# Optimization experiments

Measured on AMD Instinct MI355X. Metric: run time of the kernel, lower is better.

## Reference

```python
import jax, jax.numpy as jnp
import numpy as np

GRID_SIZE = 5
GRID_RANGE = (-1.0, 1.0)


def setup_inputs() -> dict:
    key = jax.random.key(0)
    k1, k2, k3 = jax.random.split(key, 3)
    B, D, U, K = 16384, 1024, 128, GRID_SIZE + 3  # spline_order=3
    x = jax.random.normal(k1, (B, D), dtype=jnp.float32)
    # glorot-ish scale for weights
    base_weight = jax.random.normal(k2, (D, U), dtype=jnp.float32) * (1.0 / np.sqrt(D))
    spline_weight = jax.random.normal(k3, (D, U, K), dtype=jnp.float32) * (1.0 / np.sqrt(D))
    return {"x": x, "base_weight": base_weight, "spline_weight": spline_weight}


def reference(x, base_weight, spline_weight):
    # base path: SiLU(x @ W_b)
    base_out = jax.nn.silu(x @ base_weight)  # [B, U]
    # spline path: RBF over grid centers, then contract (note: x_norm in the
    # original call() is computed but unused, so it is omitted here)
    centers = jnp.linspace(GRID_RANGE[0], GRID_RANGE[1], GRID_SIZE)  # [G]
    dist = jnp.square(x[..., None] - centers)        # [B, D, G]
    rbf = jnp.exp(-5.0 * dist)                        # [B, D, G]
    spline_out = jnp.einsum('big,iug->bu', rbf, spline_weight[:, :, :GRID_SIZE])
    return base_out + spline_out
```

## Files before the change

### kernel.cpp

```cpp
#include <hip/hip_runtime.h>

typedef unsigned short u16;
typedef unsigned int u32;
typedef __bf16 bf16x8 __attribute__((ext_vector_type(8)));
typedef float f32x16 __attribute__((ext_vector_type(16)));

#define C2 (-7.213475204444817f)
#define T1C 0.28650480f
#define T2C 0.0067379470f

__device__ __forceinline__ u16 f2bf(float f) {
  u32 u = __float_as_uint(f);
  return (u16)((u + 0x7FFFu + ((u >> 16) & 1u)) >> 16);
}

__device__ __forceinline__ f32x16 mfma16(uint4 a, uint4 b, f32x16 c) {
  return __builtin_amdgcn_mfma_f32_32x32x16_bf16(
      __builtin_bit_cast(bf16x8, a), __builtin_bit_cast(bf16x8, b), c, 0, 0, 0);
}

__global__ __launch_bounds__(256) void kan_prep(const float* __restrict__ wb,
                                                const float* __restrict__ ws,
                                                u16* __restrict__ wst3) {
  __shared__ u16 tile[6][16][130];
  const int t = threadIdx.x;
  const int c = blockIdx.x;
#pragma unroll
  for (int it = 0; it < 8; ++it) {
    int idx = it * 256 + t;
    int d = idx >> 7, u = idx & 127;
    size_t base = (size_t)(c * 16 + d) * 128 + u;
    const float* p = ws + base * 8;
    float4 v0 = *(const float4*)p;
    float g4 = p[4];
    tile[0][d][u] = f2bf(v0.x);
    tile[1][d][u] = f2bf(v0.y);
    tile[2][d][u] = f2bf(v0.z);
    tile[3][d][u] = f2bf(v0.w);
    tile[4][d][u] = f2bf(g4);
    tile[5][d][u] = f2bf(wb[base]);
  }
  __syncthreads();
#pragma unroll
  for (int i = 0; i < 6; ++i) {
    int g = i * 256 + t;
    int s = g >> 8, r = g & 255;
    int nq = r >> 6, l = r & 63;
    int u = nq * 32 + (l & 31);
    int dbase = (l >> 5) * 8;
    u32 q[4];
#pragma unroll
    for (int j = 0; j < 4; ++j) {
      u32 lo = tile[s][dbase + 2 * j][u];
      u32 hi = tile[s][dbase + 2 * j + 1][u];
      q[j] = lo | (hi << 16);
    }
    uint4 w4; w4.x = q[0]; w4.y = q[1]; w4.z = q[2]; w4.w = q[3];
    *(uint4*)(wst3 + (size_t)c * 12288 + (size_t)g * 8) = w4;
  }
}

__global__ __launch_bounds__(512, 2) void kan_main(const float* __restrict__ x,
                                                   const u16* __restrict__ wst3,
                                                   float* __restrict__ out) {
  __shared__ __align__(16) char lds[98304];

  const int t = threadIdx.x;
  const int lane = t & 63;
  const int w = t >> 6;
  const int b0 = blockIdx.x * 64;

  if (w < 4) {
    const int pid = (w << 6) + lane;
    const int r0 = pid >> 3;
    const int o = pid & 7;
    const u32 aw0 = ((u32)(o >> 1) << 10) + ((u32)(o & 1) << 9) +
                    ((u32)((r0 ^ o) & 31) << 4);
    const u32 aw1 = aw0 + 4096;
    const float* xpA = x + (size_t)(b0 + r0) * 1024 + o * 8;
    const float* xpB = xpA + 32 * 1024;

    auto rbf6 = [&](char* buf, u32 aw, float4 xa, float4 xb) {
      float xf[8] = {xa.x, xa.y, xa.z, xa.w, xb.x, xb.y, xb.z, xb.w};
      u32 pk[6][4];
#pragma unroll
      for (int pp = 0; pp < 4; ++pp) {
        u32 lo6[6], hi6[6];
#pragma unroll
        for (int e = 0; e < 2; ++e) {
          float xv = xf[2 * pp + e];
          float t0 = C2 * xv;
          float P = __builtin_amdgcn_exp2f(t0 * xv);
          float Qp = __builtin_amdgcn_exp2f(-t0);
          float Qm = __builtin_amdgcn_exp2f(t0);
          float PQ = P * Qp, PQm = P * Qm;
          u32* dst = e ? hi6 : lo6;
          dst[0] = __float_as_uint(PQm * Qm * T2C) + 0x8000u;
          dst[1] = __float_as_uint(PQm * T1C) + 0x8000u;
          dst[2] = __float_as_uint(P) + 0x8000u;
          dst[3] = __float_as_uint(PQ * T1C) + 0x8000u;
          dst[4] = __float_as_uint(PQ * Qp * T2C) + 0x8000u;
          dst[5] = __float_as_uint(xv) + 0x8000u;
        }
#pragma unroll
        for (int s = 0; s < 6; ++s)
          pk[s][pp] = __builtin_amdgcn_perm(hi6[s], lo6[s], 0x07060302);
      }
#pragma unroll
      for (int s = 0; s < 6; ++s) {
        uint4 v; v.x = pk[s][0]; v.y = pk[s][1]; v.z = pk[s][2]; v.w = pk[s][3];
        *(uint4*)(buf + s * 8192 + aw) = v;
      }
    };

    float4 xA0 = *(const float4*)(xpA);
    float4 xA1 = *(const float4*)(xpA + 4);
    float4 xB0 = *(const float4*)(xpB);
    float4 xB1 = *(const float4*)(xpB + 4);
    rbf6(lds, aw0, xA0, xA1);
    rbf6(lds, aw1, xB0, xB1);
    xA0 = *(const float4*)(xpA + 64);
    xA1 = *(const float4*)(xpA + 68);
    xB0 = *(const float4*)(xpB + 64);
    xB1 = *(const float4*)(xpB + 68);
    __syncthreads();

    for (int i = 0; i < 16; ++i) {
      if (i < 15) {
        char* nxt = lds + ((i + 1) & 1) * 49152;
        rbf6(nxt, aw0, xA0, xA1);
        rbf6(nxt, aw1, xB0, xB1);
        if (i < 14) {
          xA0 = *(const float4*)(xpA + (i + 2) * 64);
          xA1 = *(const float4*)(xpA + (i + 2) * 64 + 4);
          xB0 = *(const float4*)(xpB + (i + 2) * 64);
          xB1 = *(const float4*)(xpB + (i + 2) * 64 + 4);
        }
      }
      __syncthreads();
    }
  } else {
    const int wn = w - 4;
    const int kh = lane >> 5;
    u32 aoff[4];
#pragma unroll
    for (int p = 0; p < 4; ++p)
      aoff[p] = (u32)(p * 1024 + kh * 512 +
                      ((((lane & 31) ^ (p * 2 + kh)) & 31) << 4));
    const char* bb = (const char*)wst3 + wn * 1024 + lane * 16;

    f32x16 acc[4];
#pragma unroll
    for (int i = 0; i < 4; ++i)
#pragma unroll
      for (int j = 0; j < 16; ++j) acc[i][j] = 0.f;

    __syncthreads();

    for (int i = 0; i < 16; ++i) {
      const char* cur = lds + (i & 1) * 49152;
      uint4 bv[4][6];
#pragma unroll
      for (int p = 0; p < 4; ++p)
#pragma unroll
        for (int s = 0; s < 6; ++s)
          bv[p][s] =
              *(const uint4*)(bb + (size_t)(i * 4 + p) * 24576 + s * 4096);
#pragma unroll
      for (int p = 0; p < 4; ++p) {
        uint4 a0[6], a1[6];
#pragma unroll
        for (int s = 0; s < 6; ++s) {
          a0[s] = *(const uint4*)(cur + s * 8192 + aoff[p]);
          a1[s] = *(const uint4*)(cur + s * 8192 + 4096 + aoff[p]);
        }
        __builtin_amdgcn_s_setprio(1);
#pragma unroll
        for (int s = 0; s < 5; ++s) {
          acc[0] = mfma16(a0[s], bv[p][s], acc[0]);
          acc[1] = mfma16(a1[s], bv[p][s], acc[1]);
        }
        acc[2] = mfma16(a0[5], bv[p][5], acc[2]);
        acc[3] = mfma16(a1[5], bv[p][5], acc[3]);
        __builtin_amdgcn_s_setprio(0);
      }
      __syncthreads();
    }

    const int col = wn * 32 + (lane & 31);
#pragma unroll
    for (int g = 0; g < 2; ++g) {
#pragma unroll
      for (int reg = 0; reg < 16; ++reg) {
        int row = g * 32 + (reg & 3) + 8 * (reg >> 2) + 4 * (lane >> 5);
        float z = acc[2 + g][reg];
        float sv = z / (1.0f + __expf(-z));
        out[(size_t)(b0 + row) * 128 + col] = sv + acc[g][reg];
      }
    }
  }
}

extern "C" void kernel_launch(void* const* d_in, const int* in_sizes, int n_in,
                              void* d_out, int out_size, void* d_ws, size_t ws_size,
                              hipStream_t stream) {
  const float* x  = (const float*)d_in[0];
  const float* wb = (const float*)d_in[1];
  const float* ws = (const float*)d_in[2];
  u16* wst3 = (u16*)d_ws;
  float* out = (float*)d_out;

  kan_prep<<<dim3(64), 256, 0, stream>>>(wb, ws, wst3);
  kan_main<<<dim3(256), 512, 0, stream>>>(x, wst3, out);
}
```

Before: 124.2 us.

## Split consumer waves into 2x2 N/K tiles with triple-buffered LDS

The four MFMA waves now form a 2x2 grid. Each covers 64 output columns for half of every K-body, instead of 32 columns over the full K. Partial sums are combined through an LDS reduction before the SiLU epilogue. The producer waves now build smaller 32-column RBF bodies into six LDS slots, so three bodies are in flight at once, and LDS grows to 144KB. The aim is to raise the MFMA count per A/B fragment load and deepen the producer/consumer pipeline. In exchange, accumulator register pressure doubles to 128 floats per lane, the reduction step adds LDS traffic, and spills or lower occupancy are possible.

After: 132.8 us. +6.9%, slower.

```diff
diff --git a/kernel.cpp b/kernel.cpp
--- a/kernel.cpp
+++ b/kernel.cpp
@@ -63,7 +63,7 @@
 __global__ __launch_bounds__(512, 2) void kan_main(const float* __restrict__ x,
                                                    const u16* __restrict__ wst3,
                                                    float* __restrict__ out) {
-  __shared__ __align__(16) char lds[98304];
+  __shared__ __align__(16) char lds[147456];
 
   const int t = threadIdx.x;
   const int lane = t & 63;
@@ -71,17 +71,15 @@
   const int b0 = blockIdx.x * 64;
 
   if (w < 4) {
-    const int pid = (w << 6) + lane;
-    const int r0 = pid >> 3;
-    const int o = pid & 7;
-    const u32 aw0 = ((u32)(o >> 1) << 10) + ((u32)(o & 1) << 9) +
-                    ((u32)((r0 ^ o) & 31) << 4);
-    const u32 aw1 = aw0 + 4096;
-    const float* xpA = x + (size_t)(b0 + r0) * 1024 + o * 8;
-    const float* xpB = xpA + 32 * 1024;
-
-    auto rbf6 = [&](char* buf, u32 aw, float4 xa, float4 xb) {
-      float xf[8] = {xa.x, xa.y, xa.z, xa.w, xb.x, xb.y, xb.z, xb.w};
+    const int r = lane;
+    const int o2 = w;
+    const int g = r >> 5, m = r & 31;
+    const u32 aw = (u32)(((g * 2 + (o2 >> 1)) << 10) + ((o2 & 1) << 9) +
+                         (((m ^ o2) & 31) << 4));
+    const float* xp = x + (size_t)(b0 + r) * 1024 + o2 * 8;
+
+    auto rbf6 = [&](char* dst, float4 va, float4 vb) {
+      float xf[8] = {va.x, va.y, va.z, va.w, vb.x, vb.y, vb.z, vb.w};
       u32 pk[6][4];
 #pragma unroll
       for (int pp = 0; pp < 4; ++pp) {
@@ -94,13 +92,13 @@
           float Qp = __builtin_amdgcn_exp2f(-t0);
           float Qm = __builtin_amdgcn_exp2f(t0);
           float PQ = P * Qp, PQm = P * Qm;
-          u32* dst = e ? hi6 : lo6;
-          dst[0] = __float_as_uint(PQm * Qm * T2C) + 0x8000u;
-          dst[1] = __float_as_uint(PQm * T1C) + 0x8000u;
-          dst[2] = __float_as_uint(P) + 0x8000u;
-          dst[3] = __float_as_uint(PQ * T1C) + 0x8000u;
-          dst[4] = __float_as_uint(PQ * Qp * T2C) + 0x8000u;
-          dst[5] = __float_as_uint(xv) + 0x8000u;
+          u32* d = e ? hi6 : lo6;
+          d[0] = __float_as_uint(PQm * Qm * T2C) + 0x8000u;
+          d[1] = __float_as_uint(PQm * T1C) + 0x8000u;
+          d[2] = __float_as_uint(P) + 0x8000u;
+          d[3] = __float_as_uint(PQ * T1C) + 0x8000u;
+          d[4] = __float_as_uint(PQ * Qp * T2C) + 0x8000u;
+          d[5] = __float_as_uint(xv) + 0x8000u;
         }
 #pragma unroll
         for (int s = 0; s < 6; ++s)
@@ -109,94 +107,125 @@
 #pragma unroll
       for (int s = 0; s < 6; ++s) {
         uint4 v; v.x = pk[s][0]; v.y = pk[s][1]; v.z = pk[s][2]; v.w = pk[s][3];
-        *(uint4*)(buf + s * 8192 + aw) = v;
+        *(uint4*)(dst + s * 4096) = v;
       }
     };
 
-    float4 xA0 = *(const float4*)(xpA);
-    float4 xA1 = *(const float4*)(xpA + 4);
-    float4 xB0 = *(const float4*)(xpB);
-    float4 xB1 = *(const float4*)(xpB + 4);
-    rbf6(lds, aw0, xA0, xA1);
-    rbf6(lds, aw1, xB0, xB1);
-    xA0 = *(const float4*)(xpA + 64);
-    xA1 = *(const float4*)(xpA + 68);
-    xB0 = *(const float4*)(xpB + 64);
-    xB1 = *(const float4*)(xpB + 68);
-    __syncthreads();
-
-    for (int i = 0; i < 16; ++i) {
-      if (i < 15) {
-        char* nxt = lds + ((i + 1) & 1) * 49152;
-        rbf6(nxt, aw0, xA0, xA1);
-        rbf6(nxt, aw1, xB0, xB1);
-        if (i < 14) {
-          xA0 = *(const float4*)(xpA + (i + 2) * 64);
-          xA1 = *(const float4*)(xpA + (i + 2) * 64 + 4);
-          xB0 = *(const float4*)(xpB + (i + 2) * 64);
-          xB1 = *(const float4*)(xpB + (i + 2) * 64 + 4);
-        }
+    float4 xa = *(const float4*)xp;
+    float4 xb = *(const float4*)(xp + 4);
+    float4 na = *(const float4*)(xp + 32);
+    float4 nb = *(const float4*)(xp + 36);
+
+    auto produce = [&](int body, int slot) {
+      rbf6(lds + slot * 24576 + aw, xa, xb);
+      xa = na; xb = nb;
+      if (body + 2 < 32) {
+        na = *(const float4*)(xp + (body + 2) * 32);
+        nb = *(const float4*)(xp + (body + 2) * 32 + 4);
+      }
+    };
+
+    produce(0, 0); produce(1, 1); produce(2, 2);
+    __syncthreads();
+    for (int j = 0; j < 11; ++j) {
+      const int ps = (j & 1) ? 0 : 3;
+#pragma unroll
+      for (int bq = 0; bq < 3; ++bq) {
+        int body = 3 * j + 3 + bq;
+        if (body < 32) produce(body, ps + bq);
       }
       __syncthreads();
     }
+    __syncthreads();
   } else {
-    const int wn = w - 4;
-    const int kh = lane >> 5;
-    u32 aoff[4];
-#pragma unroll
-    for (int p = 0; p < 4; ++p)
-      aoff[p] = (u32)(p * 1024 + kh * 512 +
-                      ((((lane & 31) ^ (p * 2 + kh)) & 31) << 4));
-    const char* bb = (const char*)wst3 + wn * 1024 + lane * 16;
-
-    f32x16 acc[4];
-#pragma unroll
-    for (int i = 0; i < 4; ++i)
-#pragma unroll
-      for (int j = 0; j < 16; ++j) acc[i][j] = 0.f;
-
-    __syncthreads();
-
-    for (int i = 0; i < 16; ++i) {
-      const char* cur = lds + (i & 1) * 49152;
-      uint4 bv[4][6];
-#pragma unroll
-      for (int p = 0; p < 4; ++p)
-#pragma unroll
-        for (int s = 0; s < 6; ++s)
-          bv[p][s] =
-              *(const uint4*)(bb + (size_t)(i * 4 + p) * 24576 + s * 4096);
-#pragma unroll
-      for (int p = 0; p < 4; ++p) {
-        uint4 a0[6], a1[6];
-#pragma unroll
-        for (int s = 0; s < 6; ++s) {
-          a0[s] = *(const uint4*)(cur + s * 8192 + aoff[p]);
-          a1[s] = *(const uint4*)(cur + s * 8192 + 4096 + aoff[p]);
-        }
-        __builtin_amdgcn_s_setprio(1);
-#pragma unroll
-        for (int s = 0; s < 5; ++s) {
-          acc[0] = mfma16(a0[s], bv[p][s], acc[0]);
-          acc[1] = mfma16(a1[s], bv[p][s], acc[1]);
-        }
-        acc[2] = mfma16(a0[5], bv[p][5], acc[2]);
-        acc[3] = mfma16(a1[5], bv[p][5], acc[3]);
-        __builtin_amdgcn_s_setprio(0);
+    const int c = w - 4;
+    const int wn = c & 1;
+    const int kc = c >> 1;
+    const int m = lane & 31, hh = lane >> 5;
+    const u32 ar0 = (u32)((kc << 10) + (hh << 9) +
+                          (((m ^ (kc * 2 + hh)) & 31) << 4));
+    const u32 ar1 = ar0 + 2048;
+    const char* bb =
+        (const char*)wst3 + (size_t)kc * 24576 + wn * 2048 + lane * 16;
+
+    f32x16 acc[8];
+#pragma unroll
+    for (int i = 0; i < 8; ++i)
+#pragma unroll
+      for (int jj = 0; jj < 16; ++jj) acc[i][jj] = 0.f;
+
+    __syncthreads();
+    for (int j = 0; j < 11; ++j) {
+      const int cs = (j & 1) ? 3 : 0;
+#pragma unroll
+      for (int bq = 0; bq < 3; ++bq) {
+        int body = 3 * j + bq;
+        if (body < 32) {
+          const char* ab = lds + (cs + bq) * 24576;
+          const char* bby = bb + (size_t)body * 49152;
+#pragma unroll
+          for (int h = 0; h < 2; ++h) {
+            uint4 bv0[3], bv1[3], a0[3], a1[3];
+#pragma unroll
+            for (int si = 0; si < 3; ++si) {
+              int s = h * 3 + si;
+              bv0[si] = *(const uint4*)(bby + s * 4096);
+              bv1[si] = *(const uint4*)(bby + s * 4096 + 1024);
+              a0[si] = *(const uint4*)(ab + s * 4096 + ar0);
+              a1[si] = *(const uint4*)(ab + s * 4096 + ar1);
+            }
+            __builtin_amdgcn_s_setprio(1);
+#pragma unroll
+            for (int si = 0; si < 3; ++si) {
+              int s = h * 3 + si;
+              int bi = (s < 5) ? 0 : 4;
+              acc[bi + 0] = mfma16(a0[si], bv0[si], acc[bi + 0]);
+              acc[bi + 1] = mfma16(a0[si], bv1[si], acc[bi + 1]);
+              acc[bi + 2] = mfma16(a1[si], bv0[si], acc[bi + 2]);
+              acc[bi + 3] = mfma16(a1[si], bv1[si], acc[bi + 3]);
+            }
+            __builtin_amdgcn_s_setprio(0);
+          }
+        }
       }
       __syncthreads();
     }
 
-    const int col = wn * 32 + (lane & 31);
-#pragma unroll
-    for (int g = 0; g < 2; ++g) {
-#pragma unroll
-      for (int reg = 0; reg < 16; ++reg) {
-        int row = g * 32 + (reg & 3) + 8 * (reg >> 2) + 4 * (lane >> 5);
-        float z = acc[2 + g][reg];
-        float sv = z / (1.0f + __expf(-z));
-        out[(size_t)(b0 + row) * 128 + col] = sv + acc[g][reg];
-      }
+    if (kc == 1) {
+      char* slab = lds + wn * 32768;
+#pragma unroll
+      for (int a = 0; a < 8; ++a)
+#pragma unroll
+        for (int rq = 0; rq < 4; ++rq)
+          *(float4*)(slab + a * 4096 + rq * 1024 + lane * 16) =
+              make_float4(acc[a][4 * rq], acc[a][4 * rq + 1],
+                          acc[a][4 * rq + 2], acc[a][4 * rq + 3]);
+    }
+    __syncthreads();
+    if (kc == 0) {
+      const char* slab = lds + wn * 32768;
+#pragma unroll
+      for (int a = 0; a < 8; ++a)
+#pragma unroll
+        for (int rq = 0; rq < 4; ++rq) {
+          float4 v = *(const float4*)(slab + a * 4096 + rq * 1024 + lane * 16);
+          acc[a][4 * rq] += v.x; acc[a][4 * rq + 1] += v.y;
+          acc[a][4 * rq + 2] += v.z; acc[a][4 * rq + 3] += v.w;
+        }
+#pragma unroll
+      for (int g2 = 0; g2 < 2; ++g2)
+#pragma unroll
+        for (int nq = 0; nq < 2; ++nq) {
+          int ai = g2 * 2 + nq;
+          int col = wn * 64 + nq * 32 + (lane & 31);
+#pragma unroll
+          for (int reg = 0; reg < 16; ++reg) {
+            int row = g2 * 32 + (reg & 3) + 8 * (reg >> 2) + 4 * (lane >> 5);
+            float z = acc[4 + ai][reg];
+            float sv = z / (1.0f + __expf(-z));
+            out[(size_t)(b0 + row) * 128 + col] = sv + acc[ai][reg];
+          }
+        }
     }
   }
 }
```

## Split K across two consumer wave groups with LDS reduction

Applied to the files above, without the earlier changes.

Grows the block from 512 to 768 threads so there are 8 MFMA consumer waves instead of 4. Each pair of consumer waves splits each stage's four K sub-chunks, two apiece, and the partial accumulators are reduced through LDS before the SiLU epilogue. The aim is more MFMA parallelism per block and fewer live B-register loads per wave. The cost is an extra LDS reduction and barrier, plus launch bounds of (768,3) that may squeeze registers while the 96KB of LDS still caps occupancy.

Result: slower. 129.1 us (+3.9%).

```diff
diff --git a/kernel.cpp b/kernel.cpp
--- a/kernel.cpp
+++ b/kernel.cpp
@@ -60,7 +60,7 @@
   }
 }
 
-__global__ __launch_bounds__(512, 2) void kan_main(const float* __restrict__ x,
+__global__ __launch_bounds__(768, 3) void kan_main(const float* __restrict__ x,
                                                    const u16* __restrict__ wst3,
                                                    float* __restrict__ out) {
   __shared__ __align__(16) char lds[98304];
@@ -139,63 +139,86 @@
       }
       __syncthreads();
     }
+    __syncthreads();
   } else {
-    const int wn = w - 4;
-    const int kh = lane >> 5;
-    u32 aoff[4];
-#pragma unroll
-    for (int p = 0; p < 4; ++p)
-      aoff[p] = (u32)(p * 1024 + kh * 512 +
-                      ((((lane & 31) ^ (p * 2 + kh)) & 31) << 4));
+    const int c = w - 4;
+    const int wn = c & 3;
+    const int kc = c >> 2;
+    const int m = lane & 31, kh = lane >> 5;
+    u32 aoff[2];
+#pragma unroll
+    for (int pl = 0; pl < 2; ++pl) {
+      int p = kc * 2 + pl;
+      aoff[pl] = (u32)(p * 1024 + kh * 512 + (((m ^ (p * 2 + kh)) & 31) << 4));
+    }
     const char* bb = (const char*)wst3 + wn * 1024 + lane * 16;
 
     f32x16 acc[4];
 #pragma unroll
     for (int i = 0; i < 4; ++i)
 #pragma unroll
-      for (int j = 0; j < 16; ++j) acc[i][j] = 0.f;
+      for (int jj = 0; jj < 16; ++jj) acc[i][jj] = 0.f;
 
     __syncthreads();
 
     for (int i = 0; i < 16; ++i) {
       const char* cur = lds + (i & 1) * 49152;
-      uint4 bv[4][6];
-#pragma unroll
-      for (int p = 0; p < 4; ++p)
-#pragma unroll
-        for (int s = 0; s < 6; ++s)
-          bv[p][s] =
-              *(const uint4*)(bb + (size_t)(i * 4 + p) * 24576 + s * 4096);
-#pragma unroll
-      for (int p = 0; p < 4; ++p) {
-        uint4 a0[6], a1[6];
+      const char* bcb = bb + (size_t)(i * 4 + kc * 2) * 24576;
+#pragma unroll
+      for (int pl = 0; pl < 2; ++pl) {
+        const char* bc = bcb + (size_t)pl * 24576;
+        uint4 bv[6], a0[6], a1[6];
+#pragma unroll
+        for (int s = 0; s < 6; ++s) bv[s] = *(const uint4*)(bc + s * 4096);
 #pragma unroll
         for (int s = 0; s < 6; ++s) {
-          a0[s] = *(const uint4*)(cur + s * 8192 + aoff[p]);
-          a1[s] = *(const uint4*)(cur + s * 8192 + 4096 + aoff[p]);
+          a0[s] = *(const uint4*)(cur + s * 8192 + aoff[pl]);
+          a1[s] = *(const uint4*)(cur + s * 8192 + 4096 + aoff[pl]);
         }
         __builtin_amdgcn_s_setprio(1);
 #pragma unroll
         for (int s = 0; s < 5; ++s) {
-          acc[0] = mfma16(a0[s], bv[p][s], acc[0]);
-          acc[1] = mfma16(a1[s], bv[p][s], acc[1]);
-        }
-        acc[2] = mfma16(a0[5], bv[p][5], acc[2]);
-        acc[3] = mfma16(a1[5], bv[p][5], acc[3]);
+          acc[0] = mfma16(a0[s], bv[s], acc[0]);
+          acc[1] = mfma16(a1[s], bv[s], acc[1]);
+        }
+        acc[2] = mfma16(a0[5], bv[5], acc[2]);
+        acc[3] = mfma16(a1[5], bv[5], acc[3]);
         __builtin_amdgcn_s_setprio(0);
       }
       __syncthreads();
     }
 
-    const int col = wn * 32 + (lane & 31);
-#pragma unroll
-    for (int g = 0; g < 2; ++g) {
-#pragma unroll
-      for (int reg = 0; reg < 16; ++reg) {
-        int row = g * 32 + (reg & 3) + 8 * (reg >> 2) + 4 * (lane >> 5);
-        float z = acc[2 + g][reg];
-        float sv = z / (1.0f + __expf(-z));
-        out[(size_t)(b0 + row) * 128 + col] = sv + acc[g][reg];
+    if (kc == 1) {
+      char* slab = lds + wn * 16384;
+#pragma unroll
+      for (int a = 0; a < 4; ++a)
+#pragma unroll
+        for (int rq = 0; rq < 4; ++rq)
+          *(float4*)(slab + a * 4096 + rq * 1024 + lane * 16) =
+              make_float4(acc[a][4 * rq], acc[a][4 * rq + 1],
+                          acc[a][4 * rq + 2], acc[a][4 * rq + 3]);
+    }
+    __syncthreads();
+    if (kc == 0) {
+      const char* slab = lds + wn * 16384;
+#pragma unroll
+      for (int a = 0; a < 4; ++a)
+#pragma unroll
+        for (int rq = 0; rq < 4; ++rq) {
+          float4 v = *(const float4*)(slab + a * 4096 + rq * 1024 + lane * 16);
+          acc[a][4 * rq] += v.x; acc[a][4 * rq + 1] += v.y;
+          acc[a][4 * rq + 2] += v.z; acc[a][4 * rq + 3] += v.w;
+        }
+      const int col = wn * 32 + (lane & 31);
+#pragma unroll
+      for (int g = 0; g < 2; ++g) {
+#pragma unroll
+        for (int reg = 0; reg < 16; ++reg) {
+          int row = g * 32 + (reg & 3) + 8 * (reg >> 2) + 4 * (lane >> 5);
+          float z = acc[2 + g][reg];
+          float sv = z / (1.0f + __expf(-z));
+          out[(size_t)(b0 + row) * 128 + col] = sv + acc[g][reg];
+        }
       }
     }
   }
@@ -211,5 +234,5 @@
   float* out = (float*)d_out;
 
   kan_prep<<<dim3(64), 256, 0, stream>>>(wb, ws, wst3);
-  kan_main<<<dim3(256), 512, 0, stream>>>(x, wst3, out);
-}
+  kan_main<<<dim3(256), 768, 0, stream>>>(x, wst3, out);
+}
```

## Prefetch B-weight chunks one step ahead and use lighter split barriers

Applied to the files above, without the earlier changes.

The consumer waves now double-buffer weight loads one k-chunk ahead in registers (even/odd buffers) instead of issuing all four chunks' global loads at the start of each iteration. The block-wide __syncthreads are replaced by raw s_barrier plus a scheduling fence, with the producer side waiting only on LDS counters, so outstanding global loads are not drained at every barrier. The aim is to hide global weight-load latency behind MFMA work and cut barrier stalls. The risk is that the barrier count must still match between the two wave groups, and register pressure changes.

Result: no change. 123.9 us (-0.3%).

```diff
diff --git a/kernel.cpp b/kernel.cpp
--- a/kernel.cpp
+++ b/kernel.cpp
@@ -60,6 +60,18 @@
   }
 }
 
+#define RBAR()                            \
+  do {                                    \
+    __builtin_amdgcn_s_barrier();         \
+    __builtin_amdgcn_sched_barrier(0);    \
+  } while (0)
+#define PBAR()                                          \
+  do {                                                  \
+    asm volatile("s_waitcnt lgkmcnt(0)" ::: "memory");  \
+    __builtin_amdgcn_s_barrier();                       \
+    __builtin_amdgcn_sched_barrier(0);                  \
+  } while (0)
+
 __global__ __launch_bounds__(512, 2) void kan_main(const float* __restrict__ x,
                                                    const u16* __restrict__ wst3,
                                                    float* __restrict__ out) {
@@ -123,7 +135,7 @@
     xA1 = *(const float4*)(xpA + 68);
     xB0 = *(const float4*)(xpB + 64);
     xB1 = *(const float4*)(xpB + 68);
-    __syncthreads();
+    PBAR();
 
     for (int i = 0; i < 16; ++i) {
       if (i < 15) {
@@ -137,37 +149,44 @@
           xB1 = *(const float4*)(xpB + (i + 2) * 64 + 4);
         }
       }
-      __syncthreads();
-    }
+      PBAR();
+    }
+    __syncthreads();
   } else {
     const int wn = w - 4;
-    const int kh = lane >> 5;
+    const int m = lane & 31, kh = lane >> 5;
     u32 aoff[4];
 #pragma unroll
     for (int p = 0; p < 4; ++p)
-      aoff[p] = (u32)(p * 1024 + kh * 512 +
-                      ((((lane & 31) ^ (p * 2 + kh)) & 31) << 4));
+      aoff[p] = (u32)(p * 1024 + kh * 512 + (((m ^ (p * 2 + kh)) & 31) << 4));
     const char* bb = (const char*)wst3 + wn * 1024 + lane * 16;
 
+    auto ldB = [&](int chunk, uint4* dst) {
+      const char* bc = bb + (size_t)chunk * 24576;
+#pragma unroll
+      for (int s = 0; s < 6; ++s) dst[s] = *(const uint4*)(bc + s * 4096);
+    };
+
     f32x16 acc[4];
 #pragma unroll
     for (int i = 0; i < 4; ++i)
 #pragma unroll
-      for (int j = 0; j < 16; ++j) acc[i][j] = 0.f;
-
-    __syncthreads();
+      for (int jj = 0; jj < 16; ++jj) acc[i][jj] = 0.f;
+
+    uint4 bvE[6], bvO[6];
+    ldB(0, bvE);
+
+    RBAR();
 
     for (int i = 0; i < 16; ++i) {
       const char* cur = lds + (i & 1) * 49152;
-      uint4 bv[4][6];
-#pragma unroll
-      for (int p = 0; p < 4; ++p)
-#pragma unroll
-        for (int s = 0; s < 6; ++s)
-          bv[p][s] =
-              *(const uint4*)(bb + (size_t)(i * 4 + p) * 24576 + s * 4096);
 #pragma unroll
       for (int p = 0; p < 4; ++p) {
+        const int c = i * 4 + p;
+        uint4* bcur = (p & 1) ? bvO : bvE;
+        uint4* bnxt = (p & 1) ? bvE : bvO;
+        int cn = c + 1; if (cn > 63) cn = 63;
+        ldB(cn, bnxt);
         uint4 a0[6], a1[6];
 #pragma unroll
         for (int s = 0; s < 6; ++s) {
@@ -177,17 +196,18 @@
         __builtin_amdgcn_s_setprio(1);
 #pragma unroll
         for (int s = 0; s < 5; ++s) {
-          acc[0] = mfma16(a0[s], bv[p][s], acc[0]);
-          acc[1] = mfma16(a1[s], bv[p][s], acc[1]);
-        }
-        acc[2] = mfma16(a0[5], bv[p][5], acc[2]);
-        acc[3] = mfma16(a1[5], bv[p][5], acc[3]);
+          acc[0] = mfma16(a0[s], bcur[s], acc[0]);
+          acc[1] = mfma16(a1[s], bcur[s], acc[1]);
+        }
+        acc[2] = mfma16(a0[5], bcur[5], acc[2]);
+        acc[3] = mfma16(a1[5], bcur[5], acc[3]);
         __builtin_amdgcn_s_setprio(0);
       }
-      __syncthreads();
+      RBAR();
     }
 
     const int col = wn * 32 + (lane & 31);
+    __syncthreads();
 #pragma unroll
     for (int g = 0; g < 2; ++g) {
 #pragma unroll
```
